# Kernel tuning notes

Measured on AMD Instinct MI355X. Metric: run time of the kernel, lower is better.

## Reference

```python
import jax, jax.numpy as jnp
import numpy as np

VOCAB = 32000
DIM = 768
DEPTH = 4
D_STATE = 16
D_CONV = 4
EXPAND = 2
D_INNER = DIM * EXPAND          # 1536
DT_RANK = -(-DIM // 16)         # ceil(768/16) = 48
BATCH, SEQ = 2, 2048
EPS = 1e-5


def setup_inputs() -> dict:
    key = jax.random.key(0)
    ks = jax.random.split(key, 16)
    s = 0.02
    inp = {
        "input_ids": jax.random.randint(ks[0], (BATCH, SEQ), 0, VOCAB, dtype=jnp.int64) if jax.config.read('jax_enable_x64') else jax.random.randint(ks[0], (BATCH, SEQ), 0, VOCAB, dtype=jnp.int32),
        "emb": s * jax.random.normal(ks[1], (VOCAB, DIM), jnp.float32),
        "W_in": s * jax.random.normal(ks[2], (DEPTH, 2 * D_INNER, DIM), jnp.float32),
        "conv_w": s * jax.random.normal(ks[3], (DEPTH, D_INNER, D_CONV), jnp.float32),
        "conv_b": s * jax.random.normal(ks[4], (DEPTH, D_INNER), jnp.float32),
        "W_x": s * jax.random.normal(ks[5], (DEPTH, DT_RANK + 2 * D_STATE, D_INNER), jnp.float32),
        "W_dt": s * jax.random.normal(ks[6], (DEPTH, D_INNER, DT_RANK), jnp.float32),
        "b_dt": jnp.zeros((DEPTH, D_INNER), jnp.float32),
        "A_log": jnp.tile(jnp.log(jnp.arange(1, D_STATE + 1, dtype=jnp.float32))[None, None, :], (DEPTH, D_INNER, 1)),
        "Dp": jnp.ones((DEPTH, D_INNER), jnp.float32),
        "W_out": s * jax.random.normal(ks[7], (DEPTH, DIM, D_INNER), jnp.float32),
        "ln_g": jnp.ones((DIM,), jnp.float32),
        "ln_b": jnp.zeros((DIM,), jnp.float32),
        "W_head": s * jax.random.normal(ks[8], (VOCAB, DIM), jnp.float32),
    }
    return inp


def _mamba_block(x, W_in, conv_w, conv_b, W_x, W_dt, b_dt, A_log, Dp, W_out):
    # x: [B, L, dim]
    B_, L, _ = x.shape
    xz = x @ W_in.T                               # [B, L, 2*D_INNER]
    x_in, z = jnp.split(xz, 2, axis=-1)
    # causal depthwise conv1d (torch padding=d_conv-1 then truncate to L)
    x_pad = jnp.pad(x_in, ((0, 0), (D_CONV - 1, 0), (0, 0)))
    x_conv = conv_b + sum(x_pad[:, k:k + L, :] * conv_w[:, k] for k in range(D_CONV))
    x_ssm = jax.nn.silu(x_conv)                   # [B, L, D_INNER]
    dbl = x_ssm @ W_x.T                           # [B, L, DT_RANK + 2*D_STATE]
    dt = jax.nn.softplus(dbl[..., :DT_RANK] @ W_dt.T + b_dt)  # [B, L, D_INNER]
    Bm = dbl[..., DT_RANK:DT_RANK + D_STATE]      # [B, L, D_STATE]
    Cm = dbl[..., DT_RANK + D_STATE:]             # [B, L, D_STATE]
    A = -jnp.exp(A_log)                           # [D_INNER, D_STATE]

    def step(h, inp):
        dt_t, x_t, B_t, C_t = inp                 # [B,Din],[B,Din],[B,ds],[B,ds]
        dA = jnp.exp(dt_t[:, :, None] * A)
        h = h * dA + (dt_t * x_t)[:, :, None] * B_t[:, None, :]
        y_t = jnp.einsum('bds,bs->bd', h, C_t)
        return h, y_t

    h0 = jnp.zeros((B_, D_INNER, D_STATE), x.dtype)
    xs = (dt.transpose(1, 0, 2), x_ssm.transpose(1, 0, 2),
          Bm.transpose(1, 0, 2), Cm.transpose(1, 0, 2))
    _, ys = jax.lax.scan(step, h0, xs)            # [L, B, D_INNER]
    y = ys.transpose(1, 0, 2) + x_ssm * Dp
    return (y * jax.nn.silu(z)) @ W_out.T


def reference(input_ids, emb, W_in, conv_w, conv_b, W_x, W_dt, b_dt, A_log, Dp, W_out, ln_g, ln_b, W_head):
    x = emb[input_ids]                            # [B, L, dim]
    for i in range(DEPTH):                        # NOTE: no residual, as in source
        x = _mamba_block(x, W_in[i], conv_w[i], conv_b[i], W_x[i], W_dt[i],
                         b_dt[i], A_log[i], Dp[i], W_out[i])
    mu = jnp.mean(x, axis=-1, keepdims=True)
    var = jnp.mean(jnp.square(x - mu), axis=-1, keepdims=True)
    x = (x - mu) * jax.lax.rsqrt(var + EPS) * ln_g + ln_b
    logits = x @ W_head.T                         # [B, L, VOCAB]
    return logits
```

## Files before the change

### kernel.cpp

```cpp
#include <hip/hip_runtime.h>
#include <hip/hip_bf16.h>

#define DMODEL 768
#define DINNER 1536
#define NROWS  4096
#define SEQLEN 2048
#define DSTATE 16
#define DTRANK 48
#define DXP    80
#define NVOCAB 32000
#define TCHUNK 64
#define NCHUNK 32

typedef unsigned short u16;
typedef __attribute__((ext_vector_type(8))) short  short8;
typedef __attribute__((ext_vector_type(4))) float  floatx4;

__device__ __forceinline__ u16 f2bf(float f) {
    unsigned u = __builtin_bit_cast(unsigned, f);
    unsigned r = 0x7FFFu + ((u >> 16) & 1u);
    return (u16)((u + r) >> 16);
}
__device__ __forceinline__ float bf2f(u16 h) {
    unsigned u = ((unsigned)h) << 16;
    return __builtin_bit_cast(float, u);
}
__device__ __forceinline__ float siluf(float x) { return x / (1.f + expf(-x)); }
__device__ __forceinline__ float softplusf(float x) {
    return fmaxf(x, 0.f) + log1pf(__expf(-fabsf(x)));
}
__device__ __forceinline__ void gload_lds16(const u16* g, u16* l) {
    __builtin_amdgcn_global_load_lds((const __attribute__((address_space(1))) void*)g,
                                     (__attribute__((address_space(3))) void*)l, 16, 0, 0);
}

__global__ void k_split(const float* __restrict__ in, u16* __restrict__ hi,
                        u16* __restrict__ lo, int n4) {
    int i = blockIdx.x * blockDim.x + threadIdx.x;
    int stride = gridDim.x * blockDim.x;
    for (; i < n4; i += stride) {
        float4 f = ((const float4*)in)[i];
        u16 h0 = f2bf(f.x), h1 = f2bf(f.y), h2 = f2bf(f.z), h3 = f2bf(f.w);
        ushort4 hv; hv.x = h0; hv.y = h1; hv.z = h2; hv.w = h3;
        ((ushort4*)hi)[i] = hv;
        if (lo) {
            ushort4 lv;
            lv.x = f2bf(f.x - bf2f(h0));
            lv.y = f2bf(f.y - bf2f(h1));
            lv.z = f2bf(f.z - bf2f(h2));
            lv.w = f2bf(f.w - bf2f(h3));
            ((ushort4*)lo)[i] = lv;
        }
    }
}

__global__ void k_embed(const int* __restrict__ ids, const float* __restrict__ emb,
                        float* __restrict__ x) {
    int row = blockIdx.x;
    int id = ids[row];
    const float* src = emb + (size_t)id * DMODEL;
    float* dst = x + (size_t)row * DMODEL;
    for (int c = threadIdx.x; c < DMODEL; c += blockDim.x) dst[c] = src[c];
}

__global__ void k_conv_silu(const float* __restrict__ xz, const float* __restrict__ cw,
                            const float* __restrict__ cb, float* __restrict__ ssm,
                            float* __restrict__ sz) {
    int row = blockIdx.y;
    int d   = blockIdx.x * blockDim.x + threadIdx.x;
    int t   = row & (SEQLEN - 1);
    float acc = cb[d];
    #pragma unroll
    for (int k = 0; k < 4; ++k) {
        int tt = t + k - 3;
        if (tt >= 0) acc += xz[(size_t)(row + k - 3) * (2 * DINNER) + d] * cw[d * 4 + k];
    }
    ssm[(size_t)row * DINNER + d] = siluf(acc);
    float z = xz[(size_t)row * (2 * DINNER) + DINNER + d];
    sz[(size_t)row * DINNER + d] = siluf(z);
}

__global__ void k_softplus(float* __restrict__ dtp, const float* __restrict__ bd, int n4) {
    int i = blockIdx.x * blockDim.x + threadIdx.x;
    int stride = gridDim.x * blockDim.x;
    for (; i < n4; i += stride) {
        float4 v = ((float4*)dtp)[i];
        int d = (i * 4) % DINNER;
        float4 b = *(const float4*)&bd[d];
        v.x = softplusf(v.x + b.x);
        v.y = softplusf(v.y + b.y);
        v.z = softplusf(v.z + b.z);
        v.w = softplusf(v.w + b.w);
        ((float4*)dtp)[i] = v;
    }
}

__global__ void k_scan1(const float* __restrict__ dtp, const float* __restrict__ ssm,
                        const float* __restrict__ dbl, const float* __restrict__ Alog,
                        float* __restrict__ hend, float* __restrict__ Pout) {
    int ch   = blockIdx.x;
    int b    = blockIdx.y / (DINNER / 16);
    int dblk = blockIdx.y % (DINNER / 16);
    int dl = threadIdx.x >> 4;
    int s  = threadIdx.x & 15;
    int d  = dblk * 16 + dl;
    float A = -__expf(Alog[d * DSTATE + s]);
    float h = 0.f, P = 1.f;
    size_t row = (size_t)b * SEQLEN + (size_t)ch * TCHUNK;
    for (int t = 0; t < TCHUNK; ++t, ++row) {
        float dt = dtp[row * DINNER + d];
        float xv = ssm[row * DINNER + d];
        float Bv = dbl[row * DXP + DTRANK + s];
        float dA = __expf(dt * A);
        h = h * dA + dt * xv * Bv;
        P *= dA;
    }
    size_t o = (((size_t)b * NCHUNK + ch) * DINNER + d) * DSTATE + s;
    hend[o] = h;
    Pout[o] = P;
}

__global__ void k_scan2(const float* __restrict__ hend, const float* __restrict__ P,
                        float* __restrict__ h0) {
    int idx = blockIdx.x * blockDim.x + threadIdx.x;
    int b  = idx / (DINNER * DSTATE);
    int ds = idx % (DINNER * DSTATE);
    float h = 0.f;
    size_t base = (size_t)b * NCHUNK * DINNER * DSTATE + ds;
    for (int c = 0; c < NCHUNK; ++c) {
        size_t o = base + (size_t)c * (DINNER * DSTATE);
        h0[o] = h;
        h = hend[o] + P[o] * h;
    }
}

__global__ void k_scan3(const float* __restrict__ dtp, const float* __restrict__ ssm,
                        const float* __restrict__ dbl, const float* __restrict__ Alog,
                        const float* __restrict__ Dpv, const float* __restrict__ sz,
                        const float* __restrict__ h0, float* __restrict__ u) {
    int ch   = blockIdx.x;
    int b    = blockIdx.y / (DINNER / 16);
    int dblk = blockIdx.y % (DINNER / 16);
    int dl = threadIdx.x >> 4;
    int s  = threadIdx.x & 15;
    int d  = dblk * 16 + dl;
    float A  = -__expf(Alog[d * DSTATE + s]);
    float Dd = Dpv[d];
    float h  = h0[(((size_t)b * NCHUNK + ch) * DINNER + d) * DSTATE + s];
    size_t row = (size_t)b * SEQLEN + (size_t)ch * TCHUNK;
    for (int t = 0; t < TCHUNK; ++t, ++row) {
        float dt = dtp[row * DINNER + d];
        float xv = ssm[row * DINNER + d];
        float Bv = dbl[row * DXP + DTRANK + s];
        float Cv = dbl[row * DXP + DTRANK + DSTATE + s];
        float dA = __expf(dt * A);
        h = h * dA + dt * xv * Bv;
        float yv = h * Cv;
        yv += __shfl_xor(yv, 1);
        yv += __shfl_xor(yv, 2);
        yv += __shfl_xor(yv, 4);
        yv += __shfl_xor(yv, 8);
        if (s == 0) u[row * DINNER + d] = (yv + xv * Dd) * sz[row * DINNER + d];
    }
}

__global__ void k_ln(const float* __restrict__ x, const float* __restrict__ g,
                     const float* __restrict__ bb, u16* __restrict__ out) {
    __shared__ float red[256];
    int row = blockIdx.x;
    int tid = threadIdx.x;
    const float* xr = x + (size_t)row * DMODEL;
    float v0 = xr[tid], v1 = xr[tid + 256], v2 = xr[tid + 512];
    red[tid] = v0 + v1 + v2;
    __syncthreads();
    for (int o = 128; o > 0; o >>= 1) { if (tid < o) red[tid] += red[tid + o]; __syncthreads(); }
    float mu = red[0] * (1.f / 768.f);
    __syncthreads();
    red[tid] = (v0 - mu) * (v0 - mu) + (v1 - mu) * (v1 - mu) + (v2 - mu) * (v2 - mu);
    __syncthreads();
    for (int o = 128; o > 0; o >>= 1) { if (tid < o) red[tid] += red[tid + o]; __syncthreads(); }
    float var = red[0] * (1.f / 768.f);
    float rs = rsqrtf(var + 1e-5f);
    u16* orow = out + (size_t)row * DMODEL;
    orow[tid]       = f2bf((v0 - mu) * rs * g[tid]       + bb[tid]);
    orow[tid + 256] = f2bf((v1 - mu) * rs * g[tid + 256] + bb[tid + 256]);
    orow[tid + 512] = f2bf((v2 - mu) * rs * g[tid + 512] + bb[tid + 512]);
}

template<int SPLIT>
__global__ __launch_bounds__(256, 2)
void k_gemm(const u16* __restrict__ Ah, const u16* __restrict__ Al,
            const u16* __restrict__ Bh, const u16* __restrict__ Bl,
            float* __restrict__ C, int M, int N, int K, int lda, int ldb, int ldc) {
    constexpr int LDK = 40;
    __shared__ __align__(16) u16 sA[2][128 * LDK];
    __shared__ __align__(16) u16 sB[2][128 * LDK];
    const int tid  = threadIdx.x;
    const int m0 = blockIdx.y * 128, n0 = blockIdx.x * 128;
    const int wave = tid >> 6, lane = tid & 63;
    const int wm = (wave >> 1) * 64, wn = (wave & 1) * 64;
    const int fr = lane & 15, fq = lane >> 4;

    floatx4 acc[4][4];
    #pragma unroll
    for (int i = 0; i < 4; ++i)
        #pragma unroll
        for (int j = 0; j < 4; ++j)
            #pragma unroll
            for (int r = 0; r < 4; ++r) acc[i][j][r] = 0.f;

    for (int kt = 0; kt < K; kt += 32) {
        __syncthreads();
        #pragma unroll
        for (int half = 0; half < 2; ++half) {
            int c  = tid + half * 256;
            int rr = c >> 2;
            int ko = (c & 3) * 8;
            int gk = kt + ko;
            {
                int gm = m0 + rr;
                short8 vh = {0,0,0,0,0,0,0,0}, vl = {0,0,0,0,0,0,0,0};
                if (gm < M) {
                    const u16* p = Ah + (size_t)gm * lda + gk;
                    if (gk + 8 <= K) vh = *(const short8*)p;
                    else { for (int jj = 0; jj < 8; ++jj) if (gk + jj < K) vh[jj] = (short)p[jj]; }
                    if (SPLIT) {
                        const u16* q = Al + (size_t)gm * lda + gk;
                        if (gk + 8 <= K) vl = *(const short8*)q;
                        else { for (int jj = 0; jj < 8; ++jj) if (gk + jj < K) vl[jj] = (short)q[jj]; }
                    }
                }
                *(short8*)&sA[0][rr * LDK + ko] = vh;
                if (SPLIT) *(short8*)&sA[1][rr * LDK + ko] = vl;
            }
            {
                int gn = n0 + rr;
                short8 vh = {0,0,0,0,0,0,0,0}, vl = {0,0,0,0,0,0,0,0};
                if (gn < N) {
                    const u16* p = Bh + (size_t)gn * ldb + gk;
                    if (gk + 8 <= K) vh = *(const short8*)p;
                    else { for (int jj = 0; jj < 8; ++jj) if (gk + jj < K) vh[jj] = (short)p[jj]; }
                    if (SPLIT) {
                        const u16* q = Bl + (size_t)gn * ldb + gk;
                        if (gk + 8 <= K) vl = *(const short8*)q;
                        else { for (int jj = 0; jj < 8; ++jj) if (gk + jj < K) vl[jj] = (short)q[jj]; }
                    }
                }
                *(short8*)&sB[0][rr * LDK + ko] = vh;
                if (SPLIT) *(short8*)&sB[1][rr * LDK + ko] = vl;
            }
        }
        __syncthreads();

        short8 aH[4], bH[4];
        #pragma unroll
        for (int i = 0; i < 4; ++i) aH[i] = *(const short8*)&sA[0][(wm + i * 16 + fr) * LDK + fq * 8];
        #pragma unroll
        for (int j = 0; j < 4; ++j) bH[j] = *(const short8*)&sB[0][(wn + j * 16 + fr) * LDK + fq * 8];
        #pragma unroll
        for (int i = 0; i < 4; ++i)
            #pragma unroll
            for (int j = 0; j < 4; ++j)
                acc[i][j] = __builtin_amdgcn_mfma_f32_16x16x32_bf16(aH[i], bH[j], acc[i][j], 0, 0, 0);
        if (SPLIT) {
            short8 aL[4], bL[4];
            #pragma unroll
            for (int i = 0; i < 4; ++i) aL[i] = *(const short8*)&sA[1][(wm + i * 16 + fr) * LDK + fq * 8];
            #pragma unroll
            for (int j = 0; j < 4; ++j) bL[j] = *(const short8*)&sB[1][(wn + j * 16 + fr) * LDK + fq * 8];
            #pragma unroll
            for (int i = 0; i < 4; ++i)
                #pragma unroll
                for (int j = 0; j < 4; ++j) {
                    acc[i][j] = __builtin_amdgcn_mfma_f32_16x16x32_bf16(aL[i], bH[j], acc[i][j], 0, 0, 0);
                    acc[i][j] = __builtin_amdgcn_mfma_f32_16x16x32_bf16(aH[i], bL[j], acc[i][j], 0, 0, 0);
                }
        }
    }
    #pragma unroll
    for (int i = 0; i < 4; ++i)
        #pragma unroll
        for (int j = 0; j < 4; ++j) {
            int m = m0 + wm + i * 16 + fq * 4;
            int n = n0 + wn + j * 16 + fr;
            if (n < N) {
                #pragma unroll
                for (int r = 0; r < 4; ++r)
                    if (m + r < M) C[(size_t)(m + r) * ldc + n] = acc[i][j][r];
            }
        }
}

template<int SPLIT>
__global__ __launch_bounds__(256, 2)
void k_gemm_fast(const u16* __restrict__ Ah, const u16* __restrict__ Al,
                 const u16* __restrict__ Bh, const u16* __restrict__ Bl,
                 float* __restrict__ C, int lda, int ldb, int ldc, int K) {
    __shared__ __align__(16) u16 sA[SPLIT + 1][128 * 32];
    __shared__ __align__(16) u16 sB[SPLIT + 1][128 * 32];
    const int nx = gridDim.x;
    const int nwg = nx * gridDim.y;
    const int lin = blockIdx.y * nx + blockIdx.x;
    const int qq = nwg >> 3, rr8 = nwg & 7;
    const int xcd = lin & 7, jj = lin >> 3;
    const int swz = (xcd < rr8 ? xcd * (qq + 1) : rr8 * (qq + 1) + (xcd - rr8) * qq) + jj;
    const int n0 = (swz % nx) * 128, m0 = (swz / nx) * 128;

    const int tid  = threadIdx.x;
    const int wave = tid >> 6, lane = tid & 63;
    const int wm = (wave >> 1) * 64, wn = (wave & 1) * 64;
    const int fr = lane & 15, fq = lane >> 4;

    const int srow = (wave << 5) + (lane >> 2);
    const int scol = (((lane & 3) ^ ((lane >> 2) & 3)) << 3);
    const int ldsoff0 = (wave << 5) * 32;

    floatx4 acc[4][4];
    #pragma unroll
    for (int i = 0; i < 4; ++i)
        #pragma unroll
        for (int j = 0; j < 4; ++j)
            #pragma unroll
            for (int r = 0; r < 4; ++r) acc[i][j][r] = 0.f;

    for (int kt = 0; kt < K; kt += 32) {
        __syncthreads();
        #pragma unroll
        for (int qi = 0; qi < 2; ++qi) {
            const int row = srow + qi * 16;
            const int lo  = ldsoff0 + (qi << 4) * 32;
            gload_lds16(Ah + (size_t)(m0 + row) * lda + kt + scol, &sA[0][lo]);
            gload_lds16(Bh + (size_t)(n0 + row) * ldb + kt + scol, &sB[0][lo]);
            if constexpr (SPLIT) {
                gload_lds16(Al + (size_t)(m0 + row) * lda + kt + scol, &sA[1][lo]);
                gload_lds16(Bl + (size_t)(n0 + row) * ldb + kt + scol, &sB[1][lo]);
            }
        }
        __syncthreads();

        short8 aH[4], bH[4];
        #pragma unroll
        for (int i = 0; i < 4; ++i)
            aH[i] = *(const short8*)&sA[0][(wm + i * 16 + fr) * 32 + ((fq ^ (fr & 3)) << 3)];
        #pragma unroll
        for (int j = 0; j < 4; ++j)
            bH[j] = *(const short8*)&sB[0][(wn + j * 16 + fr) * 32 + ((fq ^ (fr & 3)) << 3)];
        #pragma unroll
        for (int i = 0; i < 4; ++i)
            #pragma unroll
            for (int j = 0; j < 4; ++j)
                acc[i][j] = __builtin_amdgcn_mfma_f32_16x16x32_bf16(aH[i], bH[j], acc[i][j], 0, 0, 0);
        if constexpr (SPLIT) {
            short8 aL[4], bL[4];
            #pragma unroll
            for (int i = 0; i < 4; ++i)
                aL[i] = *(const short8*)&sA[1][(wm + i * 16 + fr) * 32 + ((fq ^ (fr & 3)) << 3)];
            #pragma unroll
            for (int j = 0; j < 4; ++j)
                bL[j] = *(const short8*)&sB[1][(wn + j * 16 + fr) * 32 + ((fq ^ (fr & 3)) << 3)];
            #pragma unroll
            for (int i = 0; i < 4; ++i)
                #pragma unroll
                for (int j = 0; j < 4; ++j) {
                    acc[i][j] = __builtin_amdgcn_mfma_f32_16x16x32_bf16(aL[i], bH[j], acc[i][j], 0, 0, 0);
                    acc[i][j] = __builtin_amdgcn_mfma_f32_16x16x32_bf16(aH[i], bL[j], acc[i][j], 0, 0, 0);
                }
        }
    }
    #pragma unroll
    for (int i = 0; i < 4; ++i)
        #pragma unroll
        for (int j = 0; j < 4; ++j) {
            int m = m0 + wm + i * 16 + fq * 4;
            int n = n0 + wn + j * 16 + fr;
            #pragma unroll
            for (int r = 0; r < 4; ++r)
                C[(size_t)(m + r) * ldc + n] = acc[i][j][r];
        }
}

extern "C" void kernel_launch(void* const* d_in, const int* in_sizes, int n_in,
                              void* d_out, int out_size, void* d_ws, size_t ws_size,
                              hipStream_t stream) {
    const int*   ids   = (const int*)d_in[0];
    const float* emb   = (const float*)d_in[1];
    const float* W_in  = (const float*)d_in[2];
    const float* cw    = (const float*)d_in[3];
    const float* cb    = (const float*)d_in[4];
    const float* W_x   = (const float*)d_in[5];
    const float* W_dt  = (const float*)d_in[6];
    const float* b_dt  = (const float*)d_in[7];
    const float* Alog  = (const float*)d_in[8];
    const float* Dp    = (const float*)d_in[9];
    const float* W_out = (const float*)d_in[10];
    const float* ln_g  = (const float*)d_in[11];
    const float* ln_b  = (const float*)d_in[12];
    const float* W_hd  = (const float*)d_in[13];

    char* ws = (char*)d_ws;
    float* xb   = (float*)(ws + 0);
    float* xz   = (float*)(ws + 12582912);
    float* ssm  = (float*)(ws + 62914560);
    float* szb  = (float*)(ws + 88080384);
    float* dbl  = (float*)(ws + 113246208);
    u16*   Ahb  = (u16*)(ws + 114556928);
    u16*   Alb  = (u16*)(ws + 127139840);
    u16*   Bhb  = (u16*)(ws + 139722752);
    u16*   Blb  = (u16*)(ws + 144441344);
    u16*   dblh = (u16*)(ws + 149159936);
    u16*   dbll = (u16*)(ws + 149815296);

    float* dtp = xz;
    float* ub  = xz + (size_t)NROWS * DINNER;
    u16*   lnh = Ahb;
    u16*   hdh = (u16*)xz;

    float* hendb = (float*)Ahb;
    float* Pb    = (float*)Alb;
    float* h0b   = (float*)Bhb;

    k_embed<<<NROWS, 256, 0, stream>>>(ids, emb, xb);

    for (int i = 0; i < 4; ++i) {
        k_split<<<2048, 256, 0, stream>>>(xb, Ahb, Alb, NROWS * DMODEL / 4);
        k_split<<<2048, 256, 0, stream>>>(W_in + (size_t)i * 3072 * DMODEL, Bhb, Blb, 3072 * DMODEL / 4);
        k_gemm_fast<1><<<dim3(24, 32), 256, 0, stream>>>(Ahb, Alb, Bhb, Blb, xz,
                                                         DMODEL, DMODEL, 3072, DMODEL);
        k_conv_silu<<<dim3(6, NROWS), 256, 0, stream>>>(xz, cw + (size_t)i * DINNER * 4,
                                                        cb + (size_t)i * DINNER, ssm, szb);
        k_split<<<2048, 256, 0, stream>>>(ssm, Ahb, Alb, NROWS * DINNER / 4);
        k_split<<<480, 256, 0, stream>>>(W_x + (size_t)i * DXP * DINNER, Bhb, Blb, DXP * DINNER / 4);
        k_gemm<1><<<dim3(1, 32), 256, 0, stream>>>(Ahb, Alb, Bhb, Blb, dbl,
                                                   NROWS, DXP, DINNER, DINNER, DINNER, DXP);
        k_split<<<320, 256, 0, stream>>>(dbl, dblh, dbll, NROWS * DXP / 4);
        k_split<<<72, 256, 0, stream>>>(W_dt + (size_t)i * DINNER * DTRANK, Bhb, Blb, DINNER * DTRANK / 4);
        k_gemm<1><<<dim3(12, 32), 256, 0, stream>>>(dblh, dbll, Bhb, Blb, dtp,
                                                    NROWS, DINNER, DTRANK, DXP, DTRANK, DINNER);
        k_softplus<<<2048, 256, 0, stream>>>(dtp, b_dt + (size_t)i * DINNER, NROWS * DINNER / 4);
        k_scan1<<<dim3(NCHUNK, 2 * (DINNER / 16)), 256, 0, stream>>>(
            dtp, ssm, dbl, Alog + (size_t)i * DINNER * DSTATE, hendb, Pb);
        k_scan2<<<192, 256, 0, stream>>>(hendb, Pb, h0b);
        k_scan3<<<dim3(NCHUNK, 2 * (DINNER / 16)), 256, 0, stream>>>(
            dtp, ssm, dbl, Alog + (size_t)i * DINNER * DSTATE,
            Dp + (size_t)i * DINNER, szb, h0b, ub);
        k_split<<<2048, 256, 0, stream>>>(ub, Ahb, Alb, NROWS * DINNER / 4);
        k_split<<<2048, 256, 0, stream>>>(W_out + (size_t)i * DMODEL * DINNER, Bhb, Blb, DMODEL * DINNER / 4);
        k_gemm_fast<1><<<dim3(6, 32), 256, 0, stream>>>(Ahb, Alb, Bhb, Blb, xb,
                                                        DINNER, DINNER, DMODEL, DINNER);
    }

    k_ln<<<NROWS, 256, 0, stream>>>(xb, ln_g, ln_b, lnh);
    k_split<<<8192, 256, 0, stream>>>(W_hd, hdh, (u16*)nullptr, NVOCAB * DMODEL / 4);
    k_gemm_fast<0><<<dim3(250, 32), 256, 0, stream>>>(lnh, nullptr, hdh, nullptr, (float*)d_out,
                                                      DMODEL, DMODEL, NVOCAB, DMODEL);
}
```

Baseline: 2.915 ms.

## Fuse bf16 hi/lo splits into producers, split-K the x-projection, fuse softplus

The bf16 hi/lo split of activations now happens inside the producing kernels (embed, conv+silu, scan3, out-proj GEMM epilogue), so the separate split passes over large fp32 buffers go away. The narrow x-projection GEMM (N=80), which before ran on only 32 blocks, becomes a split-K kernel across 8 K-slices plus a reduce kernel, giving more parallelism. Softplus with bias moves into the dt GEMM epilogue. The cost is extra writes of partial sums, and the scans now read two u16 arrays instead of one fp32 array.

```diff
diff --git a/kernel.cpp b/kernel.cpp
--- a/kernel.cpp
+++ b/kernel.cpp
@@ -11,6 +11,7 @@
 #define NVOCAB 32000
 #define TCHUNK 64
 #define NCHUNK 32
+#define KSPLIT 8
 
 typedef unsigned short u16;
 typedef __attribute__((ext_vector_type(8))) short  short8;
@@ -55,17 +56,25 @@
 }
 
 __global__ void k_embed(const int* __restrict__ ids, const float* __restrict__ emb,
-                        float* __restrict__ x) {
+                        float* __restrict__ x, u16* __restrict__ xh, u16* __restrict__ xl) {
     int row = blockIdx.x;
     int id = ids[row];
     const float* src = emb + (size_t)id * DMODEL;
     float* dst = x + (size_t)row * DMODEL;
-    for (int c = threadIdx.x; c < DMODEL; c += blockDim.x) dst[c] = src[c];
+    u16* dh = xh + (size_t)row * DMODEL;
+    u16* dl = xl + (size_t)row * DMODEL;
+    for (int c = threadIdx.x; c < DMODEL; c += blockDim.x) {
+        float v = src[c];
+        dst[c] = v;
+        u16 h = f2bf(v);
+        dh[c] = h;
+        dl[c] = f2bf(v - bf2f(h));
+    }
 }
 
 __global__ void k_conv_silu(const float* __restrict__ xz, const float* __restrict__ cw,
-                            const float* __restrict__ cb, float* __restrict__ ssm,
-                            float* __restrict__ sz) {
+                            const float* __restrict__ cb, u16* __restrict__ ssmh,
+                            u16* __restrict__ ssml, float* __restrict__ sz) {
     int row = blockIdx.y;
     int d   = blockIdx.x * blockDim.x + threadIdx.x;
     int t   = row & (SEQLEN - 1);
@@ -75,28 +84,18 @@
         int tt = t + k - 3;
         if (tt >= 0) acc += xz[(size_t)(row + k - 3) * (2 * DINNER) + d] * cw[d * 4 + k];
     }
-    ssm[(size_t)row * DINNER + d] = siluf(acc);
+    float s = siluf(acc);
+    u16 h = f2bf(s);
+    size_t o = (size_t)row * DINNER + d;
+    ssmh[o] = h;
+    ssml[o] = f2bf(s - bf2f(h));
     float z = xz[(size_t)row * (2 * DINNER) + DINNER + d];
-    sz[(size_t)row * DINNER + d] = siluf(z);
-}
-
-__global__ void k_softplus(float* __restrict__ dtp, const float* __restrict__ bd, int n4) {
-    int i = blockIdx.x * blockDim.x + threadIdx.x;
-    int stride = gridDim.x * blockDim.x;
-    for (; i < n4; i += stride) {
-        float4 v = ((float4*)dtp)[i];
-        int d = (i * 4) % DINNER;
-        float4 b = *(const float4*)&bd[d];
-        v.x = softplusf(v.x + b.x);
-        v.y = softplusf(v.y + b.y);
-        v.z = softplusf(v.z + b.z);
-        v.w = softplusf(v.w + b.w);
-        ((float4*)dtp)[i] = v;
-    }
-}
-
-__global__ void k_scan1(const float* __restrict__ dtp, const float* __restrict__ ssm,
-                        const float* __restrict__ dbl, const float* __restrict__ Alog,
+    sz[o] = siluf(z);
+}
+
+__global__ void k_scan1(const float* __restrict__ dtp, const u16* __restrict__ ssmh,
+                        const u16* __restrict__ ssml, const float* __restrict__ dbl,
+                        const float* __restrict__ Alog,
                         float* __restrict__ hend, float* __restrict__ Pout) {
     int ch   = blockIdx.x;
     int b    = blockIdx.y / (DINNER / 16);
@@ -109,7 +108,7 @@
     size_t row = (size_t)b * SEQLEN + (size_t)ch * TCHUNK;
     for (int t = 0; t < TCHUNK; ++t, ++row) {
         float dt = dtp[row * DINNER + d];
-        float xv = ssm[row * DINNER + d];
+        float xv = bf2f(ssmh[row * DINNER + d]) + bf2f(ssml[row * DINNER + d]);
         float Bv = dbl[row * DXP + DTRANK + s];
         float dA = __expf(dt * A);
         h = h * dA + dt * xv * Bv;
@@ -134,10 +133,11 @@
     }
 }
 
-__global__ void k_scan3(const float* __restrict__ dtp, const float* __restrict__ ssm,
-                        const float* __restrict__ dbl, const float* __restrict__ Alog,
-                        const float* __restrict__ Dpv, const float* __restrict__ sz,
-                        const float* __restrict__ h0, float* __restrict__ u) {
+__global__ void k_scan3(const float* __restrict__ dtp, const u16* __restrict__ ssmh,
+                        const u16* __restrict__ ssml, const float* __restrict__ dbl,
+                        const float* __restrict__ Alog, const float* __restrict__ Dpv,
+                        const float* __restrict__ sz, const float* __restrict__ h0,
+                        u16* __restrict__ uh, u16* __restrict__ ul) {
     int ch   = blockIdx.x;
     int b    = blockIdx.y / (DINNER / 16);
     int dblk = blockIdx.y % (DINNER / 16);
@@ -150,7 +150,7 @@
     size_t row = (size_t)b * SEQLEN + (size_t)ch * TCHUNK;
     for (int t = 0; t < TCHUNK; ++t, ++row) {
         float dt = dtp[row * DINNER + d];
-        float xv = ssm[row * DINNER + d];
+        float xv = bf2f(ssmh[row * DINNER + d]) + bf2f(ssml[row * DINNER + d]);
         float Bv = dbl[row * DXP + DTRANK + s];
         float Cv = dbl[row * DXP + DTRANK + DSTATE + s];
         float dA = __expf(dt * A);
@@ -160,7 +160,12 @@
         yv += __shfl_xor(yv, 2);
         yv += __shfl_xor(yv, 4);
         yv += __shfl_xor(yv, 8);
-        if (s == 0) u[row * DINNER + d] = (yv + xv * Dd) * sz[row * DINNER + d];
+        if (s == 0) {
+            float val = (yv + xv * Dd) * sz[row * DINNER + d];
+            u16 hh = f2bf(val);
+            uh[row * DINNER + d] = hh;
+            ul[row * DINNER + d] = f2bf(val - bf2f(hh));
+        }
     }
 }
 
@@ -187,11 +192,12 @@
     orow[tid + 512] = f2bf((v2 - mu) * rs * g[tid + 512] + bb[tid + 512]);
 }
 
-template<int SPLIT>
+template<int SPLIT, int EPI>
 __global__ __launch_bounds__(256, 2)
 void k_gemm(const u16* __restrict__ Ah, const u16* __restrict__ Al,
             const u16* __restrict__ Bh, const u16* __restrict__ Bl,
-            float* __restrict__ C, int M, int N, int K, int lda, int ldb, int ldc) {
+            float* __restrict__ C, const float* __restrict__ bias,
+            int M, int N, int K, int lda, int ldb, int ldc) {
     constexpr int LDK = 40;
     __shared__ __align__(16) u16 sA[2][128 * LDK];
     __shared__ __align__(16) u16 sB[2][128 * LDK];
@@ -286,16 +292,21 @@
             if (n < N) {
                 #pragma unroll
                 for (int r = 0; r < 4; ++r)
-                    if (m + r < M) C[(size_t)(m + r) * ldc + n] = acc[i][j][r];
+                    if (m + r < M) {
+                        float v = acc[i][j][r];
+                        if (EPI) v = softplusf(v + bias[n]);
+                        C[(size_t)(m + r) * ldc + n] = v;
+                    }
             }
         }
 }
 
-template<int SPLIT>
+template<int SPLIT, int EPI>
 __global__ __launch_bounds__(256, 2)
 void k_gemm_fast(const u16* __restrict__ Ah, const u16* __restrict__ Al,
                  const u16* __restrict__ Bh, const u16* __restrict__ Bl,
-                 float* __restrict__ C, int lda, int ldb, int ldc, int K) {
+                 float* __restrict__ C, u16* __restrict__ Ch, u16* __restrict__ Cl,
+                 int lda, int ldb, int ldc, int K) {
     __shared__ __align__(16) u16 sA[SPLIT + 1][128 * 32];
     __shared__ __align__(16) u16 sB[SPLIT + 1][128 * 32];
     const int nx = gridDim.x;
@@ -374,9 +385,107 @@
             int m = m0 + wm + i * 16 + fq * 4;
             int n = n0 + wn + j * 16 + fr;
             #pragma unroll
+            for (int r = 0; r < 4; ++r) {
+                float v = acc[i][j][r];
+                C[(size_t)(m + r) * ldc + n] = v;
+                if constexpr (EPI) {
+                    u16 h = f2bf(v);
+                    Ch[(size_t)(m + r) * ldc + n] = h;
+                    Cl[(size_t)(m + r) * ldc + n] = f2bf(v - bf2f(h));
+                }
+            }
+        }
+}
+
+__global__ __launch_bounds__(256, 2)
+void k_xproj(const u16* __restrict__ Ah, const u16* __restrict__ Al,
+             const u16* __restrict__ Bh, const u16* __restrict__ Bl,
+             float* __restrict__ part) {
+    __shared__ __align__(16) u16 sA[2][128 * 32];
+    __shared__ __align__(16) u16 sB[2][128 * 32];
+    const int ks = blockIdx.x;
+    const int m0 = blockIdx.y * 128;
+    const int k0 = ks * (DINNER / KSPLIT);
+    const int tid  = threadIdx.x;
+    const int wave = tid >> 6, lane = tid & 63;
+    const int wm = wave * 32;
+    const int fr = lane & 15, fq = lane >> 4;
+    const int srow = (wave << 5) + (lane >> 2);
+    const int scol = (((lane & 3) ^ ((lane >> 2) & 3)) << 3);
+    const int ldsoff0 = (wave << 5) * 32;
+
+    floatx4 acc[2][5];
+    #pragma unroll
+    for (int i = 0; i < 2; ++i)
+        #pragma unroll
+        for (int j = 0; j < 5; ++j)
+            #pragma unroll
+            for (int r = 0; r < 4; ++r) acc[i][j][r] = 0.f;
+
+    for (int kt = 0; kt < DINNER / KSPLIT; kt += 32) {
+        __syncthreads();
+        #pragma unroll
+        for (int qi = 0; qi < 2; ++qi) {
+            const int row = srow + qi * 16;
+            const int lo  = ldsoff0 + (qi << 4) * 32;
+            gload_lds16(Ah + (size_t)(m0 + row) * DINNER + k0 + kt + scol, &sA[0][lo]);
+            gload_lds16(Al + (size_t)(m0 + row) * DINNER + k0 + kt + scol, &sA[1][lo]);
+            gload_lds16(Bh + (size_t)row * DINNER + k0 + kt + scol, &sB[0][lo]);
+            gload_lds16(Bl + (size_t)row * DINNER + k0 + kt + scol, &sB[1][lo]);
+        }
+        __syncthreads();
+
+        short8 aH[2], aL[2], bH[5], bL[5];
+        #pragma unroll
+        for (int i = 0; i < 2; ++i) {
+            aH[i] = *(const short8*)&sA[0][(wm + i * 16 + fr) * 32 + ((fq ^ (fr & 3)) << 3)];
+            aL[i] = *(const short8*)&sA[1][(wm + i * 16 + fr) * 32 + ((fq ^ (fr & 3)) << 3)];
+        }
+        #pragma unroll
+        for (int j = 0; j < 5; ++j) {
+            bH[j] = *(const short8*)&sB[0][(j * 16 + fr) * 32 + ((fq ^ (fr & 3)) << 3)];
+            bL[j] = *(const short8*)&sB[1][(j * 16 + fr) * 32 + ((fq ^ (fr & 3)) << 3)];
+        }
+        #pragma unroll
+        for (int i = 0; i < 2; ++i)
+            #pragma unroll
+            for (int j = 0; j < 5; ++j) {
+                acc[i][j] = __builtin_amdgcn_mfma_f32_16x16x32_bf16(aH[i], bH[j], acc[i][j], 0, 0, 0);
+                acc[i][j] = __builtin_amdgcn_mfma_f32_16x16x32_bf16(aL[i], bH[j], acc[i][j], 0, 0, 0);
+                acc[i][j] = __builtin_amdgcn_mfma_f32_16x16x32_bf16(aH[i], bL[j], acc[i][j], 0, 0, 0);
+            }
+    }
+    #pragma unroll
+    for (int i = 0; i < 2; ++i)
+        #pragma unroll
+        for (int j = 0; j < 5; ++j) {
+            int m = m0 + wm + i * 16 + fq * 4;
+            int n = j * 16 + fr;
+            #pragma unroll
             for (int r = 0; r < 4; ++r)
-                C[(size_t)(m + r) * ldc + n] = acc[i][j][r];
-        }
+                part[((size_t)ks * NROWS + m + r) * DXP + n] = acc[i][j][r];
+        }
+}
+
+__global__ void k_xreduce(const float* __restrict__ part, float* __restrict__ dbl,
+                          u16* __restrict__ dh, u16* __restrict__ dl) {
+    int i = blockIdx.x * blockDim.x + threadIdx.x;
+    float4 s = ((const float4*)part)[i];
+    #pragma unroll
+    for (int ks = 1; ks < KSPLIT; ++ks) {
+        float4 p = ((const float4*)(part + (size_t)ks * NROWS * DXP))[i];
+        s.x += p.x; s.y += p.y; s.z += p.z; s.w += p.w;
+    }
+    ((float4*)dbl)[i] = s;
+    u16 h0 = f2bf(s.x), h1 = f2bf(s.y), h2 = f2bf(s.z), h3 = f2bf(s.w);
+    ushort4 hv; hv.x = h0; hv.y = h1; hv.z = h2; hv.w = h3;
+    ushort4 lv;
+    lv.x = f2bf(s.x - bf2f(h0));
+    lv.y = f2bf(s.y - bf2f(h1));
+    lv.z = f2bf(s.z - bf2f(h2));
+    lv.w = f2bf(s.w - bf2f(h3));
+    ((ushort4*)dh)[i] = hv;
+    ((ushort4*)dl)[i] = lv;
 }
 
 extern "C" void kernel_launch(void* const* d_in, const int* in_sizes, int n_in,
@@ -398,59 +507,60 @@
     const float* W_hd  = (const float*)d_in[13];
 
     char* ws = (char*)d_ws;
-    float* xb   = (float*)(ws + 0);
-    float* xz   = (float*)(ws + 12582912);
-    float* ssm  = (float*)(ws + 62914560);
-    float* szb  = (float*)(ws + 88080384);
-    float* dbl  = (float*)(ws + 113246208);
-    u16*   Ahb  = (u16*)(ws + 114556928);
-    u16*   Alb  = (u16*)(ws + 127139840);
-    u16*   Bhb  = (u16*)(ws + 139722752);
-    u16*   Blb  = (u16*)(ws + 144441344);
-    u16*   dblh = (u16*)(ws + 149159936);
-    u16*   dbll = (u16*)(ws + 149815296);
+    float* xb    = (float*)(ws + 0);
+    float* xz    = (float*)(ws + 12582912);
+    float* szb   = (float*)(ws + 62914560);
+    u16*   ssmh  = (u16*)(ws + 88080384);
+    u16*   ssml  = (u16*)(ws + 100663296);
+    u16*   xAh   = (u16*)(ws + 113246208);
+    u16*   xAl   = (u16*)(ws + 119537664);
+    u16*   Bhb   = (u16*)(ws + 125829120);
+    u16*   Blb   = (u16*)(ws + 130547712);
+    u16*   Wxh   = (u16*)(ws + 135266304);
+    u16*   Wxl   = (u16*)(ws + 135512064);
+    float* dbl   = (float*)(ws + 135757824);
+    u16*   dblh  = (u16*)(ws + 137068544);
+    u16*   dbll  = (u16*)(ws + 137723904);
+    float* xpart = (float*)(ws + 138379264);
 
     float* dtp = xz;
-    float* ub  = xz + (size_t)NROWS * DINNER;
-    u16*   lnh = Ahb;
-    u16*   hdh = (u16*)xz;
-
-    float* hendb = (float*)Ahb;
-    float* Pb    = (float*)Alb;
-    float* h0b   = (float*)Bhb;
-
-    k_embed<<<NROWS, 256, 0, stream>>>(ids, emb, xb);
+    u16*   uhb = (u16*)(ws + 37748736);
+    u16*   ulb = (u16*)(ws + 50331648);
+    float* hendb = xpart;
+    float* Pb    = (float*)Bhb;
+    float* h0b   = (float*)xAh;
+    u16* lnh = ssmh;
+    u16* hdh = (u16*)xz;
+
+    k_embed<<<NROWS, 256, 0, stream>>>(ids, emb, xb, xAh, xAl);
 
     for (int i = 0; i < 4; ++i) {
-        k_split<<<2048, 256, 0, stream>>>(xb, Ahb, Alb, NROWS * DMODEL / 4);
         k_split<<<2048, 256, 0, stream>>>(W_in + (size_t)i * 3072 * DMODEL, Bhb, Blb, 3072 * DMODEL / 4);
-        k_gemm_fast<1><<<dim3(24, 32), 256, 0, stream>>>(Ahb, Alb, Bhb, Blb, xz,
-                                                         DMODEL, DMODEL, 3072, DMODEL);
+        k_gemm_fast<1, 0><<<dim3(24, 32), 256, 0, stream>>>(xAh, xAl, Bhb, Blb, xz, nullptr, nullptr,
+                                                            DMODEL, DMODEL, 3072, DMODEL);
         k_conv_silu<<<dim3(6, NROWS), 256, 0, stream>>>(xz, cw + (size_t)i * DINNER * 4,
-                                                        cb + (size_t)i * DINNER, ssm, szb);
-        k_split<<<2048, 256, 0, stream>>>(ssm, Ahb, Alb, NROWS * DINNER / 4);
-        k_split<<<480, 256, 0, stream>>>(W_x + (size_t)i * DXP * DINNER, Bhb, Blb, DXP * DINNER / 4);
-        k_gemm<1><<<dim3(1, 32), 256, 0, stream>>>(Ahb, Alb, Bhb, Blb, dbl,
-                                                   NROWS, DXP, DINNER, DINNER, DINNER, DXP);
-        k_split<<<320, 256, 0, stream>>>(dbl, dblh, dbll, NROWS * DXP / 4);
+                                                        cb + (size_t)i * DINNER, ssmh, ssml, szb);
+        k_split<<<120, 256, 0, stream>>>(W_x + (size_t)i * DXP * DINNER, Wxh, Wxl, DXP * DINNER / 4);
+        k_xproj<<<dim3(KSPLIT, 32), 256, 0, stream>>>(ssmh, ssml, Wxh, Wxl, xpart);
+        k_xreduce<<<320, 256, 0, stream>>>(xpart, dbl, dblh, dbll);
         k_split<<<72, 256, 0, stream>>>(W_dt + (size_t)i * DINNER * DTRANK, Bhb, Blb, DINNER * DTRANK / 4);
-        k_gemm<1><<<dim3(12, 32), 256, 0, stream>>>(dblh, dbll, Bhb, Blb, dtp,
-                                                    NROWS, DINNER, DTRANK, DXP, DTRANK, DINNER);
-        k_softplus<<<2048, 256, 0, stream>>>(dtp, b_dt + (size_t)i * DINNER, NROWS * DINNER / 4);
+        k_gemm<1, 1><<<dim3(12, 32), 256, 0, stream>>>(dblh, dbll, Bhb, Blb, dtp,
+                                                       b_dt + (size_t)i * DINNER,
+                                                       NROWS, DINNER, DTRANK, DXP, DTRANK, DINNER);
         k_scan1<<<dim3(NCHUNK, 2 * (DINNER / 16)), 256, 0, stream>>>(
-            dtp, ssm, dbl, Alog + (size_t)i * DINNER * DSTATE, hendb, Pb);
+            dtp, ssmh, ssml, dbl, Alog + (size_t)i * DINNER * DSTATE, hendb, Pb);
         k_scan2<<<192, 256, 0, stream>>>(hendb, Pb, h0b);
         k_scan3<<<dim3(NCHUNK, 2 * (DINNER / 16)), 256, 0, stream>>>(
-            dtp, ssm, dbl, Alog + (size_t)i * DINNER * DSTATE,
-            Dp + (size_t)i * DINNER, szb, h0b, ub);
-        k_split<<<2048, 256, 0, stream>>>(ub, Ahb, Alb, NROWS * DINNER / 4);
-        k_split<<<2048, 256, 0, stream>>>(W_out + (size_t)i * DMODEL * DINNER, Bhb, Blb, DMODEL * DINNER / 4);
-        k_gemm_fast<1><<<dim3(6, 32), 256, 0, stream>>>(Ahb, Alb, Bhb, Blb, xb,
-                                                        DINNER, DINNER, DMODEL, DINNER);
+            dtp, ssmh, ssml, dbl, Alog + (size_t)i * DINNER * DSTATE,
+            Dp + (size_t)i * DINNER, szb, h0b, uhb, ulb);
+        k_split<<<1152, 256, 0, stream>>>(W_out + (size_t)i * DMODEL * DINNER, Bhb, Blb, DMODEL * DINNER / 4);
+        k_gemm_fast<1, 1><<<dim3(6, 32), 256, 0, stream>>>(uhb, ulb, Bhb, Blb, xb, xAh, xAl,
+                                                           DINNER, DINNER, DMODEL, DINNER);
     }
 
     k_ln<<<NROWS, 256, 0, stream>>>(xb, ln_g, ln_b, lnh);
     k_split<<<8192, 256, 0, stream>>>(W_hd, hdh, (u16*)nullptr, NVOCAB * DMODEL / 4);
-    k_gemm_fast<0><<<dim3(250, 32), 256, 0, stream>>>(lnh, nullptr, hdh, nullptr, (float*)d_out,
-                                                      DMODEL, DMODEL, NVOCAB, DMODEL);
-}
+    k_gemm_fast<0, 0><<<dim3(250, 32), 256, 0, stream>>>(lnh, nullptr, hdh, nullptr, (float*)d_out,
+                                                         nullptr, nullptr,
+                                                         DMODEL, DMODEL, NVOCAB, DMODEL);
+}
```

Measured after the change: 2.663 ms. -8.6%, faster.
